# Kernel tuning notes

Hardware: AMD Instinct MI355X
Metric: run time of the kernel (lower is better)

## Reference

```python
import jax, jax.numpy as jnp
import numpy as np

N_ENT, N_USR, C, E, NNZ, NREL, NHOPS = 150000, 60000, 64, 1000000, 1000000, 10, 2
EPS = 1e-12  # torch F.normalize default eps


def setup_inputs() -> dict:
    key = jax.random.key(0)
    ks = jax.random.split(key, 8)
    return {
        "user_emb": jax.random.normal(ks[0], (N_USR, C), dtype=jnp.float32),
        "entity_emb": jax.random.normal(ks[1], (N_ENT, C), dtype=jnp.float32),
        "weight": jax.random.normal(ks[2], (NREL - 1, C), dtype=jnp.float32) * 0.1,  # xavier-ish
        "inter_vals": jax.random.uniform(ks[3], (NNZ,), dtype=jnp.float32),
        "edge_index": jax.random.randint(ks[4], (2, E), 0, N_ENT),
        "edge_type": jax.random.randint(ks[5], (E,), 0, NREL - 1),
        "inter_rows": jax.random.randint(ks[6], (NNZ,), 0, N_USR),
        "inter_cols": jax.random.randint(ks[7], (NNZ,), 0, N_ENT),
    }


def _l2_normalize(x):
    n = jnp.sqrt(jnp.sum(x * x, axis=1, keepdims=True))
    return x / jnp.maximum(n, EPS)


def _hop(entity_emb, user_emb, head, tail, edge_type, weight,
         inter_rows, inter_cols, inter_vals):
    rel = weight[edge_type - 1]                      # [E, C]
    h = entity_emb[head]                             # [E, C]
    t = entity_emb[tail]                             # [E, C]
    neigh = t * rel                                  # [E, C]
    # calculate_sim_hrt: (||h*r||_2 * ||t*r||_2)^2, per-edge scalar
    hn = jnp.linalg.norm(h * rel, axis=1)            # [E]
    tn = jnp.linalg.norm(t * rel, axis=1)            # [E]
    att = (hn * tn) ** 2                             # [E]
    # scatter_softmax over groups of `head` (value identical across channels)
    m = jax.ops.segment_max(att, head, num_segments=N_ENT)
    e = jnp.exp(att - m[head])
    s = jax.ops.segment_sum(e, head, num_segments=N_ENT)
    w = e / s[head]                                  # [E]
    entity_agg = jax.ops.segment_sum(w[:, None] * neigh, head, num_segments=N_ENT)
    # entity_agg += interact_mat.T @ user_emb
    entity_agg = entity_agg + jax.ops.segment_sum(
        inter_vals[:, None] * user_emb[inter_rows], inter_cols, num_segments=N_ENT)
    # user_agg = interact_mat @ entity_emb
    user_agg = jax.ops.segment_sum(
        inter_vals[:, None] * entity_emb[inter_cols], inter_rows, num_segments=N_USR)
    return entity_agg, user_agg


def reference(user_emb, entity_emb, weight, inter_vals,
              edge_index, edge_type, inter_rows, inter_cols):
    head, tail = edge_index[0], edge_index[1]
    ent_res, usr_res = entity_emb, user_emb
    ent, usr = entity_emb, user_emb
    for _ in range(NHOPS):
        ent, usr = _hop(ent, usr, head, tail, edge_type, weight,
                        inter_rows, inter_cols, inter_vals)
        ent = _l2_normalize(ent)  # mess_dropout disabled (eval path)
        usr = _l2_normalize(usr)
        ent_res = ent_res + ent
        usr_res = usr_res + usr
    return ent_res, usr_res
```

## Files before the change

kernel.cpp:

```cpp
#include <hip/hip_runtime.h>
#include <hip/hip_fp16.h>
#include <math.h>

#define N_ENT  150000
#define N_USR  60000
#define CDIM   64
#define NE     1000000
#define NNZV   1000000
#define NREL9  9
#define NTOT   (2 * N_ENT + N_USR)
#define TOTAL_ITEMS (NE + 2 * NNZV)
#define SCAN_B ((NTOT + 1023) / 1024)

#define NXCD   8
#define H_PER  (N_ENT / NXCD)
#define R_PER  (N_USR / NXCD)
#define EPB    2048
#define NCHUNK ((NE + EPB - 1) / EPB)

#define EG (N_ENT / 4)
#define UG (N_USR / 4)
#define UCVT ((N_USR * CDIM / 2 + 255) / 256)

#define SLICE_K 16384
#define SH 10
#define SC 10
#define SR 4
#define NSLICE (SH + SC + SR)
#define ESPLIT 8
#define ECH (NE / ESPLIT)
#define HIST_BLKS (NSLICE * ESPLIT)
#define RB ((NTOT + 255) / 256)

template <int CTRL>
__device__ __forceinline__ float dpp_addf(float v) {
    int iv = __float_as_int(v);
    int x = __builtin_amdgcn_update_dpp(iv, iv, CTRL, 0xF, 0xF, true);
    return v + __int_as_float(x);
}
template <int CTRL>
__device__ __forceinline__ float dpp_maxf(float v) {
    int iv = __float_as_int(v);
    int x = __builtin_amdgcn_update_dpp(iv, iv, CTRL, 0xF, 0xF, true);
    return fmaxf(v, __int_as_float(x));
}
__device__ __forceinline__ float wave_sum(float v) {
    v = dpp_addf<0x111>(v);
    v = dpp_addf<0x112>(v);
    v = dpp_addf<0x114>(v);
    v = dpp_addf<0x118>(v);
    v = dpp_addf<0x142>(v);
    v = dpp_addf<0x143>(v);
    return __int_as_float(__builtin_amdgcn_readlane(__float_as_int(v), 63));
}
__device__ __forceinline__ float wave_max(float v) {
    v = dpp_maxf<0x111>(v);
    v = dpp_maxf<0x112>(v);
    v = dpp_maxf<0x114>(v);
    v = dpp_maxf<0x118>(v);
    v = dpp_maxf<0x142>(v);
    v = dpp_maxf<0x143>(v);
    return __int_as_float(__builtin_amdgcn_readlane(__float_as_int(v), 63));
}

__device__ __forceinline__ float bcast_f(float v, int l) { return __int_as_float(__builtin_amdgcn_readlane(__float_as_int(v), l)); }

__device__ __forceinline__ int block_excl_scan(int v, int* lds) {
    int lane = threadIdx.x & 63, wid = threadIdx.x >> 6;
    int incl = v;
#pragma unroll
    for (int o = 1; o < 64; o <<= 1) {
        int t = __shfl_up(incl, o, 64);
        if (lane >= o) incl += t;
    }
    if (lane == 63) lds[wid] = incl;
    __syncthreads();
    int nw = blockDim.x >> 6;
    if ((int)threadIdx.x < nw) {
        int s = lds[threadIdx.x];
        int si = s;
        for (int o = 1; o < nw; o <<= 1) {
            int t = __shfl_up(si, o, 64);
            if ((int)threadIdx.x >= o) si += t;
        }
        lds[threadIdx.x] = si - s;
    }
    __syncthreads();
    return incl - v + lds[wid];
}

__global__ __launch_bounds__(256) void k_hist_lds(
    const int* __restrict__ head, const int* __restrict__ cols,
    const int* __restrict__ rows, int* __restrict__ priv)
{
    __shared__ int h[SLICE_K];
    int sid = blockIdx.x >> 3, chunk = blockIdx.x & (ESPLIT - 1);
    const int* key; int k0;
    if (sid < SH)            { key = head; k0 = sid * SLICE_K; }
    else if (sid < SH + SC)  { key = cols; k0 = (sid - SH) * SLICE_K; }
    else                     { key = rows; k0 = (sid - SH - SC) * SLICE_K; }
    for (int t = threadIdx.x; t < SLICE_K; t += 256) h[t] = 0;
    __syncthreads();
    const int4* key4 = (const int4*)(key + chunk * ECH);
    for (int i = threadIdx.x; i < ECH / 4; i += 256) {
        int4 k4 = key4[i];
        int a = k4.x - k0, b = k4.y - k0, c = k4.z - k0, d = k4.w - k0;
        if ((unsigned)a < (unsigned)SLICE_K) atomicAdd(&h[a], 1);
        if ((unsigned)b < (unsigned)SLICE_K) atomicAdd(&h[b], 1);
        if ((unsigned)c < (unsigned)SLICE_K) atomicAdd(&h[c], 1);
        if ((unsigned)d < (unsigned)SLICE_K) atomicAdd(&h[d], 1);
    }
    __syncthreads();
    int* dst = priv + (size_t)blockIdx.x * SLICE_K;
    for (int t = threadIdx.x; t < SLICE_K; t += 256) dst[t] = h[t];
}

__global__ __launch_bounds__(256) void k_prepreduce(
    const int* __restrict__ priv, int* __restrict__ cnt,
    const float* __restrict__ ent, const float* __restrict__ usr,
    const float* __restrict__ wt,
    __half* __restrict__ ent16, __half* __restrict__ usr16,
    float* __restrict__ sq)
{
    int b = blockIdx.x;
    if (b < RB) {
        int i = b * 256 + (int)threadIdx.x;
        if (i >= NTOT) return;
        int sid, local;
        if (i < N_ENT)          { sid = i >> 14;                    local = i & (SLICE_K - 1); }
        else if (i < 2 * N_ENT) { int j = i - N_ENT;     sid = SH + (j >> 14);      local = j & (SLICE_K - 1); }
        else                    { int j = i - 2 * N_ENT; sid = SH + SC + (j >> 14); local = j & (SLICE_K - 1); }
        const int* p = priv + (size_t)(sid * ESPLIT) * SLICE_K + local;
        int s = 0;
#pragma unroll
        for (int c = 0; c < ESPLIT; ++c) s += p[(size_t)c * SLICE_K];
        cnt[i] = s;
    } else if (b < RB + EG) {
        int e = ((b - RB) * 256 + (int)threadIdx.x) >> 6;
        int lane = threadIdx.x & 63;
        float own = ent[(e << 6) + lane];
        ent16[(e << 6) + lane] = __float2half(own);
        float o2 = own * own;
        float mine = 0.f;
#pragma unroll
        for (int rt = 0; rt < NREL9; ++rt) {
            float r = wt[(rt << 6) + lane];
            float s = wave_sum(o2 * r * r);
            if (lane == rt) mine = s;
        }
        if (lane < NREL9) sq[e * NREL9 + lane] = mine;
    } else {
        int i = (b - RB - EG) * 256 + (int)threadIdx.x;
        if (i < N_USR * CDIM / 2) {
            float2 v = ((const float2*)usr)[i];
            ((__half2*)usr16)[i] = __floats2half2_rn(v.x, v.y);
        }
    }
}

__global__ __launch_bounds__(1024) void k_bsum(
    const int* __restrict__ cnt, int* __restrict__ bsum)
{
    __shared__ int lds[16];
    int i = blockIdx.x * 1024 + threadIdx.x;
    float v = (i < NTOT) ? (float)cnt[i] : 0.f;
    float s = wave_sum(v);
    int lane = threadIdx.x & 63, wid = threadIdx.x >> 6;
    if (lane == 0) lds[wid] = (int)s;
    __syncthreads();
    if (threadIdx.x == 0) {
        int t = 0;
        for (int k = 0; k < 16; ++k) t += lds[k];
        bsum[blockIdx.x] = t;
    }
}

__global__ __launch_bounds__(512) void k_scan_small(int* __restrict__ bsum)
{
    __shared__ int lds[16];
    int i = threadIdx.x;
    int v = (i < SCAN_B) ? bsum[i] : 0;
    int e = block_excl_scan(v, lds);
    if (i < SCAN_B) bsum[i] = e;
}

__global__ __launch_bounds__(1024) void k_scan_apply(
    const int* __restrict__ cnt, const int* __restrict__ bsum,
    int* __restrict__ start, int* __restrict__ cursor)
{
    __shared__ int lds[16];
    int i = blockIdx.x * 1024 + threadIdx.x;
    int v = (i < NTOT) ? cnt[i] : 0;
    int e = block_excl_scan(v, lds) + bsum[blockIdx.x];
    if (i < NTOT) { start[i] = e; cursor[i] = e; }
    else if (i == NTOT) { start[i] = TOTAL_ITEMS; }
}

__global__ __launch_bounds__(256) void k_scatter(
    const int* __restrict__ head, const int* __restrict__ tail,
    const int* __restrict__ etype,
    const int* __restrict__ rows, const int* __restrict__ cols,
    const float* __restrict__ vals,
    int* __restrict__ cursor,
    int* __restrict__ pk_h,
    int2* __restrict__ rc,
    int2* __restrict__ cv)
{
    int role  = blockIdx.x & (NXCD - 1);
    int chunk = blockIdx.x >> 3;
    int h0 = role * H_PER, h1 = h0 + H_PER;
    int r0 = role * R_PER, r1 = r0 + R_PER;
    int base = chunk * EPB;
    int end  = min(base + EPB, NE);
    for (int i = base + (int)threadIdx.x; i < end; i += 256) {
        int h = head[i];
        int c = cols[i];
        int r = rows[i];
        if (h >= h0 && h < h1) {
            int rt = etype[i] - 1;
            if (rt < 0) rt = 8;
            int p = atomicAdd(cursor + h, 1);
            if ((unsigned)p < (unsigned)NE) pk_h[p] = tail[i] | (rt << 18);
        }
        if (c >= h0 && c < h1) {
            int vb = __float_as_int(vals[i]);
            int p = atomicAdd(cursor + N_ENT + c, 1) - NE;
            if ((unsigned)p < (unsigned)NNZV) rc[p] = make_int2(r, vb);
        }
        if (r >= r0 && r < r1) {
            int vb = __float_as_int(vals[i]);
            int p = atomicAdd(cursor + 2 * N_ENT + r, 1) - 2 * NE;
            if ((unsigned)p < (unsigned)NNZV) cv[p] = make_int2(c, vb);
        }
    }
}

template <bool FIRST, bool LAST>
__global__ __launch_bounds__(256) void k_hop(
    const __half* __restrict__ ent16_cur, const __half* __restrict__ usr16_cur,
    const float* __restrict__ ent_res_base, const float* __restrict__ usr_res_base,
    const float* __restrict__ wt, const int* __restrict__ start,
    const int* __restrict__ pk_h, const float* __restrict__ sq_in,
    const int2* __restrict__ rc, const int2* __restrict__ cv,
    __half* __restrict__ ent16_next, __half* __restrict__ usr16_next,
    float* __restrict__ sq_out,
    float* __restrict__ out_ent, float* __restrict__ out_usr)
{
    int lane = threadIdx.x & 63;
    int b = blockIdx.x;

    if (b < EG) {
        int e = __builtin_amdgcn_readfirstlane((b * 256 + (int)threadIdx.x) >> 6);

        int s1 = min(start[e + 1], NE);
        int s0 = min(start[e], s1);
        float m = 0.f, l = 0.f, acc = 0.f;
        for (int base = s0; base < s1; base += 64) {
            int j = base + lane;
            int cnt = min(64, s1 - base);
            float att = 0.f;
            if (j < s1) {
                int pk = pk_h[j];
                int t = pk & 0x3FFFF, rt = (pk >> 18) & 15;
                att = sq_in[e * NREL9 + rt] * sq_in[t * NREL9 + rt];
            }
            float mn = fmaxf(m, wave_max(att));
            float scale = __expf(m - mn);
            float p = (j < s1) ? __expf(att - mn) : 0.f;
            l = l * scale + wave_sum(p);
            acc *= scale;
            m = mn;
            int k = 0;
            for (; k + 4 <= cnt; k += 4) {
#pragma unroll
                for (int q = 0; q < 4; ++q) {
                    int pkk = pk_h[base + k + q];
                    float wk = bcast_f(p, k + q);
                    const __half* tp = ent16_cur + ((pkk & 0x3FFFF) << 6);
                    const float*  wp = wt + (((pkk >> 18) & 15) << 6);
                    acc += wk * __half2float(tp[lane]) * wp[lane];
                }
            }
            for (; k < cnt; ++k) {
                int pkk = pk_h[base + k];
                float wk = bcast_f(p, k);
                const __half* tp = ent16_cur + ((pkk & 0x3FFFF) << 6);
                const float*  wp = wt + (((pkk >> 18) & 15) << 6);
                acc += wk * __half2float(tp[lane]) * wp[lane];
            }
        }
        float agg = (l > 0.f) ? acc / l : 0.f;

        int c1 = min(start[N_ENT + e + 1] - NE, NNZV);
        int c0 = max(min(start[N_ENT + e] - NE, c1), 0);
        {
            int k = c0;
            for (; k + 4 <= c1; k += 4) {
#pragma unroll
                for (int q = 0; q < 4; ++q) {
                    int2 t2 = rc[k + q];
                    agg += __int_as_float(t2.y) *
                           __half2float(usr16_cur[(t2.x << 6) + lane]);
                }
            }
            for (; k < c1; ++k) {
                int2 t2 = rc[k];
                agg += __int_as_float(t2.y) *
                       __half2float(usr16_cur[(t2.x << 6) + lane]);
            }
        }

        float s = wave_sum(agg * agg);
        float y = agg / fmaxf(sqrtf(s), 1e-12f);
        int oi = (e << 6) + lane;
        if (!LAST) {
            ent16_next[oi] = __float2half(y);
            float y2 = y * y;
            float mine = 0.f;
#pragma unroll
            for (int rt = 0; rt < NREL9; ++rt) {
                float r = wt[(rt << 6) + lane];
                float sv = wave_sum(y2 * r * r);
                if (lane == rt) mine = sv;
            }
            if (lane < NREL9) sq_out[e * NREL9 + lane] = mine;
        }
        if (FIRST) out_ent[oi] = ent_res_base[oi] + y;
        else       out_ent[oi] += y;
    } else {
        int u = __builtin_amdgcn_readfirstlane(((b - EG) * 256 + (int)threadIdx.x) >> 6);
        int s1 = min(start[2 * N_ENT + u + 1] - 2 * NE, NNZV);
        int s0 = max(min(start[2 * N_ENT + u] - 2 * NE, s1), 0);
        float accA = 0.f, accB = 0.f;
        {
            int k = s0;
            for (; k + 4 <= s1; k += 4) {
#pragma unroll
                for (int q = 0; q < 4; ++q) {
                    int2 t2 = cv[k + q];
                    float prod = __int_as_float(t2.y) *
                                 __half2float(ent16_cur[(t2.x << 6) + lane]);
                    if (q & 1) accB += prod; else accA += prod;
                }
            }
            for (; k < s1; ++k) {
                int2 t2 = cv[k];
                accA += __int_as_float(t2.y) *
                        __half2float(ent16_cur[(t2.x << 6) + lane]);
            }
        }
        float acc = accA + accB;
        float s = wave_sum(acc * acc);
        float y = acc / fmaxf(sqrtf(s), 1e-12f);
        int oi = (u << 6) + lane;
        if (!LAST) usr16_next[oi] = __float2half(y);
        if (FIRST) out_usr[oi] = usr_res_base[oi] + y;
        else       out_usr[oi] += y;
    }
}

extern "C" void kernel_launch(void* const* d_in, const int* in_sizes, int n_in,
                              void* d_out, int out_size, void* d_ws, size_t ws_size,
                              hipStream_t stream)
{
    const float* user_emb   = (const float*)d_in[0];
    const float* entity_emb = (const float*)d_in[1];
    const float* wt         = (const float*)d_in[2];
    const float* inter_vals = (const float*)d_in[3];
    const int*   edge_index = (const int*)d_in[4];
    const int*   etype      = (const int*)d_in[5];
    const int*   inter_rows = (const int*)d_in[6];
    const int*   inter_cols = (const int*)d_in[7];
    const int* head  = edge_index;
    const int* tailp = edge_index + NE;

    __half* ent16_a = (__half*)d_ws;
    __half* ent16_b = ent16_a + (size_t)N_ENT * CDIM;
    __half* usr16_a = ent16_b + (size_t)N_ENT * CDIM;
    __half* usr16_b = usr16_a + (size_t)N_USR * CDIM;
    int2*  rc     = (int2*)(usr16_b + (size_t)N_USR * CDIM);
    int2*  cv     = rc + NNZV;
    int*   pk_h   = (int*)(cv + NNZV);
    int*   cnt    = pk_h + NE;
    int*   start  = cnt + NTOT;
    int*   cursor = start + NTOT + 1;
    int*   bsum   = cursor + NTOT + 1;
    float* sq_a   = (float*)(bsum + SCAN_B);
    float* sq_b   = sq_a + (size_t)N_ENT * NREL9;
    int* priv = (int*)ent16_b;

    float* out_ent = (float*)d_out;
    float* out_usr = out_ent + (size_t)N_ENT * CDIM;

    k_hist_lds<<<HIST_BLKS, 256, 0, stream>>>(head, inter_cols, inter_rows, priv);
    k_prepreduce<<<RB + EG + UCVT, 256, 0, stream>>>(
        priv, cnt, entity_emb, user_emb, wt, ent16_a, usr16_a, sq_a);
    k_bsum<<<SCAN_B, 1024, 0, stream>>>(cnt, bsum);
    k_scan_small<<<1, 512, 0, stream>>>(bsum);
    k_scan_apply<<<SCAN_B, 1024, 0, stream>>>(cnt, bsum, start, cursor);
    k_scatter<<<NCHUNK * NXCD, 256, 0, stream>>>(
        head, tailp, etype, inter_rows, inter_cols, inter_vals,
        cursor, pk_h, rc, cv);

    k_hop<true, false><<<EG + UG, 256, 0, stream>>>(
        ent16_a, usr16_a, entity_emb, user_emb, wt, start, pk_h, sq_a, rc, cv,
        ent16_b, usr16_b, sq_b, out_ent, out_usr);

    k_hop<false, true><<<EG + UG, 256, 0, stream>>>(
        ent16_b, usr16_b, nullptr, nullptr, wt, start, pk_h, sq_b, rc, cv,
        nullptr, nullptr, nullptr, out_ent, out_usr);
}
```

Baseline: 625.5 us.

## Replace global-atomic CSR scatter with LDS-slice scatter using per-chunk histogram offsets

The histogram kernel's per-chunk private counts are turned into exclusive per-chunk prefix offsets. A new scatter kernel uses the same slice-by-chunk decomposition: it seeds an LDS cursor array from the global start plus these offsets and places items with LDS atomics instead of global atomics on a cursor array. The edge split is doubled to 16 chunks and the workspace is reordered so the larger private buffer fits in the contiguous ent16_b/usr16_b region. The cost is that every scatter block re-reads its whole chunk of keys to filter its slice, and more private histogram memory is written and read.

```diff
diff --git a/kernel.cpp b/kernel.cpp
--- a/kernel.cpp
+++ b/kernel.cpp
@@ -12,12 +12,6 @@
 #define TOTAL_ITEMS (NE + 2 * NNZV)
 #define SCAN_B ((NTOT + 1023) / 1024)
 
-#define NXCD   8
-#define H_PER  (N_ENT / NXCD)
-#define R_PER  (N_USR / NXCD)
-#define EPB    2048
-#define NCHUNK ((NE + EPB - 1) / EPB)
-
 #define EG (N_ENT / 4)
 #define UG (N_USR / 4)
 #define UCVT ((N_USR * CDIM / 2 + 255) / 256)
@@ -27,7 +21,7 @@
 #define SC 10
 #define SR 4
 #define NSLICE (SH + SC + SR)
-#define ESPLIT 8
+#define ESPLIT 16
 #define ECH (NE / ESPLIT)
 #define HIST_BLKS (NSLICE * ESPLIT)
 #define RB ((NTOT + 255) / 256)
@@ -94,7 +88,7 @@
     const int* __restrict__ rows, int* __restrict__ priv)
 {
     __shared__ int h[SLICE_K];
-    int sid = blockIdx.x >> 3, chunk = blockIdx.x & (ESPLIT - 1);
+    int sid = blockIdx.x >> 4, chunk = blockIdx.x & (ESPLIT - 1);
     const int* key; int k0;
     if (sid < SH)            { key = head; k0 = sid * SLICE_K; }
     else if (sid < SH + SC)  { key = cols; k0 = (sid - SH) * SLICE_K; }
@@ -116,7 +110,7 @@
 }
 
 __global__ __launch_bounds__(256) void k_prepreduce(
-    const int* __restrict__ priv, int* __restrict__ cnt,
+    int* __restrict__ priv, int* __restrict__ cnt,
     const float* __restrict__ ent, const float* __restrict__ usr,
     const float* __restrict__ wt,
     __half* __restrict__ ent16, __half* __restrict__ usr16,
@@ -130,10 +124,14 @@
         if (i < N_ENT)          { sid = i >> 14;                    local = i & (SLICE_K - 1); }
         else if (i < 2 * N_ENT) { int j = i - N_ENT;     sid = SH + (j >> 14);      local = j & (SLICE_K - 1); }
         else                    { int j = i - 2 * N_ENT; sid = SH + SC + (j >> 14); local = j & (SLICE_K - 1); }
-        const int* p = priv + (size_t)(sid * ESPLIT) * SLICE_K + local;
+        int* p = priv + (size_t)(sid * ESPLIT) * SLICE_K + local;
         int s = 0;
 #pragma unroll
-        for (int c = 0; c < ESPLIT; ++c) s += p[(size_t)c * SLICE_K];
+        for (int c = 0; c < ESPLIT; ++c) {
+            int t = p[(size_t)c * SLICE_K];
+            p[(size_t)c * SLICE_K] = s;
+            s += t;
+        }
         cnt[i] = s;
     } else if (b < RB + EG) {
         int e = ((b - RB) * 256 + (int)threadIdx.x) >> 6;
@@ -186,51 +184,76 @@
 
 __global__ __launch_bounds__(1024) void k_scan_apply(
     const int* __restrict__ cnt, const int* __restrict__ bsum,
-    int* __restrict__ start, int* __restrict__ cursor)
+    int* __restrict__ start)
 {
     __shared__ int lds[16];
     int i = blockIdx.x * 1024 + threadIdx.x;
     int v = (i < NTOT) ? cnt[i] : 0;
     int e = block_excl_scan(v, lds) + bsum[blockIdx.x];
-    if (i < NTOT) { start[i] = e; cursor[i] = e; }
-    else if (i == NTOT) { start[i] = TOTAL_ITEMS; }
-}
-
-__global__ __launch_bounds__(256) void k_scatter(
+    if (i < NTOT) start[i] = e;
+    else if (i == NTOT) start[i] = TOTAL_ITEMS;
+}
+
+__global__ __launch_bounds__(256) void k_scatter_lds(
     const int* __restrict__ head, const int* __restrict__ tail,
     const int* __restrict__ etype,
     const int* __restrict__ rows, const int* __restrict__ cols,
     const float* __restrict__ vals,
-    int* __restrict__ cursor,
+    const int* __restrict__ start, const int* __restrict__ priv,
     int* __restrict__ pk_h,
     int2* __restrict__ rc,
     int2* __restrict__ cv)
 {
-    int role  = blockIdx.x & (NXCD - 1);
-    int chunk = blockIdx.x >> 3;
-    int h0 = role * H_PER, h1 = h0 + H_PER;
-    int r0 = role * R_PER, r1 = r0 + R_PER;
-    int base = chunk * EPB;
-    int end  = min(base + EPB, NE);
-    for (int i = base + (int)threadIdx.x; i < end; i += 256) {
-        int h = head[i];
-        int c = cols[i];
-        int r = rows[i];
-        if (h >= h0 && h < h1) {
-            int rt = etype[i] - 1;
-            if (rt < 0) rt = 8;
-            int p = atomicAdd(cursor + h, 1);
-            if ((unsigned)p < (unsigned)NE) pk_h[p] = tail[i] | (rt << 18);
-        }
-        if (c >= h0 && c < h1) {
-            int vb = __float_as_int(vals[i]);
-            int p = atomicAdd(cursor + N_ENT + c, 1) - NE;
-            if ((unsigned)p < (unsigned)NNZV) rc[p] = make_int2(r, vb);
-        }
-        if (r >= r0 && r < r1) {
-            int vb = __float_as_int(vals[i]);
-            int p = atomicAdd(cursor + 2 * N_ENT + r, 1) - 2 * NE;
-            if ((unsigned)p < (unsigned)NNZV) cv[p] = make_int2(c, vb);
+    __shared__ int cur[SLICE_K];
+    int sid = blockIdx.x >> 4, chunk = blockIdx.x & (ESPLIT - 1);
+    const int* poff = priv + (size_t)(sid * ESPLIT + chunk) * SLICE_K;
+    int e0 = chunk * ECH, e1 = e0 + ECH;
+
+    if (sid < SH) {
+        int k0 = sid * SLICE_K;
+        for (int t = threadIdx.x; t < SLICE_K; t += 256) {
+            int g = k0 + t;
+            cur[t] = (g < N_ENT) ? (start[g] + poff[t]) : 0;
+        }
+        __syncthreads();
+        for (int i = e0 + (int)threadIdx.x; i < e1; i += 256) {
+            int a = head[i] - k0;
+            if ((unsigned)a < (unsigned)SLICE_K) {
+                int rt = etype[i] - 1;
+                if (rt < 0) rt = 8;
+                int p = atomicAdd(&cur[a], 1);
+                if ((unsigned)p < (unsigned)NE) pk_h[p] = tail[i] | (rt << 18);
+            }
+        }
+    } else if (sid < SH + SC) {
+        int k0 = (sid - SH) * SLICE_K;
+        for (int t = threadIdx.x; t < SLICE_K; t += 256) {
+            int g = k0 + t;
+            cur[t] = (g < N_ENT) ? (start[N_ENT + g] - NE + poff[t]) : 0;
+        }
+        __syncthreads();
+        for (int i = e0 + (int)threadIdx.x; i < e1; i += 256) {
+            int a = cols[i] - k0;
+            if ((unsigned)a < (unsigned)SLICE_K) {
+                int p = atomicAdd(&cur[a], 1);
+                if ((unsigned)p < (unsigned)NNZV)
+                    rc[p] = make_int2(rows[i], __float_as_int(vals[i]));
+            }
+        }
+    } else {
+        int k0 = (sid - SH - SC) * SLICE_K;
+        for (int t = threadIdx.x; t < SLICE_K; t += 256) {
+            int g = k0 + t;
+            cur[t] = (g < N_USR) ? (start[2 * N_ENT + g] - 2 * NE + poff[t]) : 0;
+        }
+        __syncthreads();
+        for (int i = e0 + (int)threadIdx.x; i < e1; i += 256) {
+            int a = rows[i] - k0;
+            if ((unsigned)a < (unsigned)SLICE_K) {
+                int p = atomicAdd(&cur[a], 1);
+                if ((unsigned)p < (unsigned)NNZV)
+                    cv[p] = make_int2(cols[i], __float_as_int(vals[i]));
+            }
         }
     }
 }
@@ -375,19 +398,18 @@
     const int* tailp = edge_index + NE;
 
     __half* ent16_a = (__half*)d_ws;
-    __half* ent16_b = ent16_a + (size_t)N_ENT * CDIM;
-    __half* usr16_a = ent16_b + (size_t)N_ENT * CDIM;
-    __half* usr16_b = usr16_a + (size_t)N_USR * CDIM;
+    __half* usr16_a = ent16_a + (size_t)N_ENT * CDIM;
+    __half* ent16_b = usr16_a + (size_t)N_USR * CDIM;
+    __half* usr16_b = ent16_b + (size_t)N_ENT * CDIM;
     int2*  rc     = (int2*)(usr16_b + (size_t)N_USR * CDIM);
     int2*  cv     = rc + NNZV;
     int*   pk_h   = (int*)(cv + NNZV);
     int*   cnt    = pk_h + NE;
     int*   start  = cnt + NTOT;
-    int*   cursor = start + NTOT + 1;
-    int*   bsum   = cursor + NTOT + 1;
+    int*   bsum   = start + NTOT + 1;
     float* sq_a   = (float*)(bsum + SCAN_B);
     float* sq_b   = sq_a + (size_t)N_ENT * NREL9;
-    int* priv = (int*)ent16_b;
+    int*   priv   = (int*)ent16_b;
 
     float* out_ent = (float*)d_out;
     float* out_usr = out_ent + (size_t)N_ENT * CDIM;
@@ -397,10 +419,10 @@
         priv, cnt, entity_emb, user_emb, wt, ent16_a, usr16_a, sq_a);
     k_bsum<<<SCAN_B, 1024, 0, stream>>>(cnt, bsum);
     k_scan_small<<<1, 512, 0, stream>>>(bsum);
-    k_scan_apply<<<SCAN_B, 1024, 0, stream>>>(cnt, bsum, start, cursor);
-    k_scatter<<<NCHUNK * NXCD, 256, 0, stream>>>(
+    k_scan_apply<<<SCAN_B, 1024, 0, stream>>>(cnt, bsum, start);
+    k_scatter_lds<<<HIST_BLKS, 256, 0, stream>>>(
         head, tailp, etype, inter_rows, inter_cols, inter_vals,
-        cursor, pk_h, rc, cv);
+        start, priv, pk_h, rc, cv);
 
     k_hop<true, false><<<EG + UG, 256, 0, stream>>>(
         ent16_a, usr16_a, entity_emb, user_emb, wt, start, pk_h, sq_a, rc, cv,
```

New measurement: 682.9 us. +9.2%, slower.
